# Kernel optimization log

Measured on AMD Instinct MI355X. Metric: run time of the kernel, lower is better.

Reference implementation:

```python
import jax, jax.numpy as jnp
import numpy as np

N = 1024   # num_nodes
D = 128    # embedding_size


def setup_inputs() -> dict:
    key = jax.random.key(0)
    k1, k2, k3 = jax.random.split(key, 3)
    z = jax.random.normal(k1, (N, D), dtype=jnp.float32)
    # torch.nn.Linear(2D, D): weight [D, 2D]; stored here as W1 [2D, D] for x @ W1
    W1 = jax.random.normal(k2, (2 * D, D), dtype=jnp.float32) * (1.0 / np.sqrt(2 * D))
    b1 = jnp.zeros((D,), dtype=jnp.float32)
    W2 = jax.random.normal(k3, (D, 1), dtype=jnp.float32) * (1.0 / np.sqrt(D))
    b2 = jnp.zeros((1,), dtype=jnp.float32)
    return {"z": z, "W1": W1, "b1": b1, "W2": W2, "b2": b2}


def reference(z, W1, b1, W2, b2):
    # Original: z_i = z.repeat_interleave(N) (i varies slowly),
    #           z_j = z.repeat(N)            (j varies fast),
    # q = Linear2(relu(Linear1(cat[z_i, z_j]))).squeeze()  -> shape [N*N]
    # Equivalent split-linear form (cat @ W1 == z_i @ W1[:D] + z_j @ W1[D:]):
    d = z.shape[1]
    pi = z @ W1[:d]          # [N, D] projection of left node
    pj = z @ W1[d:]          # [N, D] projection of right node
    h = jax.nn.relu(pi[:, None, :] + pj[None, :, :] + b1)  # [N, N, D]
    q = (h @ W2).squeeze(-1) + b2                          # [N, N]
    return q.reshape(-1)     # pair k = i*N + j, matching repeat_interleave/repeat order
```

## Files before the change

### kernel.cpp

```cpp
#include <hip/hip_runtime.h>


#define NN 1024
#define DD 128
#define TI 64
#define TJ 32
#define PAD 132

__global__ __launch_bounds__(256) void proj_kernel(
    const float* __restrict__ z,
    const float* __restrict__ W1,
    const float* __restrict__ b1,
    float* __restrict__ pic,
    float* __restrict__ pj)
{
    const int i0 = blockIdx.x * 4;
    const int t = threadIdx.x;
    const int half = t >> 7;
    const int d = t & (DD - 1);
    const float* __restrict__ Wcol = W1 + half * DD * DD + d;
    const float* __restrict__ z0 = z + i0 * DD;

    float a0 = 0.f, a1 = 0.f, a2 = 0.f, a3 = 0.f;
    #pragma unroll 8
    for (int k = 0; k < DD; ++k) {
        const float w = Wcol[k * DD];
        a0 = fmaf(z0[k], w, a0);
        a1 = fmaf(z0[DD + k], w, a1);
        a2 = fmaf(z0[2 * DD + k], w, a2);
        a3 = fmaf(z0[3 * DD + k], w, a3);
    }
    if (half == 0) {
        const float bb = b1[d];
        pic[(i0 + 0) * DD + d] = a0 + bb;
        pic[(i0 + 1) * DD + d] = a1 + bb;
        pic[(i0 + 2) * DD + d] = a2 + bb;
        pic[(i0 + 3) * DD + d] = a3 + bb;
    } else {
        pj[(i0 + 0) * DD + d] = a0;
        pj[(i0 + 1) * DD + d] = a1;
        pj[(i0 + 2) * DD + d] = a2;
        pj[(i0 + 3) * DD + d] = a3;
    }
}

__global__ __launch_bounds__(256, 2) void pair_kernel(
    const float* __restrict__ pic,
    const float* __restrict__ pj,
    const float* __restrict__ W2,
    const float* __restrict__ b2,
    float* __restrict__ out)
{
    __shared__ float a_s[TI * PAD];
    __shared__ float b_s[TJ * PAD];

    const int t  = threadIdx.x;
    const int bi = blockIdx.x;
    const int bj = blockIdx.y;

    const float4* __restrict__ srcA = (const float4*)(pic + bi * TI * DD);
    const float4* __restrict__ srcB = (const float4*)(pj + bj * TJ * DD);
    #pragma unroll
    for (int u = 0; u < 8; ++u) {
        int f   = t + 256 * u;
        int row = f >> 5;
        int c4  = f & 31;
        *(float4*)&a_s[row * PAD + c4 * 4] = srcA[f];
    }
    #pragma unroll
    for (int u = 0; u < 4; ++u) {
        int f   = t + 256 * u;
        int row = f >> 5;
        int c4  = f & 31;
        *(float4*)&b_s[row * PAD + c4 * 4] = srcB[f];
    }
    __syncthreads();

    const int tx = t & 15;
    const int ty = t >> 4;
    const float* ap = a_s + ty * PAD;
    const float* bp = b_s + tx * PAD;

    float acc[4][2];
    #pragma unroll
    for (int ii = 0; ii < 4; ++ii)
        #pragma unroll
        for (int jj = 0; jj < 2; ++jj) acc[ii][jj] = 0.f;

    #pragma unroll
    for (int d = 0; d < DD; d += 4) {
        const float4 w4 = *(const float4*)(W2 + d);
        float4 av[4], bv[2];
        #pragma unroll
        for (int ii = 0; ii < 4; ++ii) av[ii] = *(const float4*)(ap + ii * 16 * PAD + d);
        #pragma unroll
        for (int jj = 0; jj < 2; ++jj) bv[jj] = *(const float4*)(bp + jj * 16 * PAD + d);

        #pragma unroll
        for (int ii = 0; ii < 4; ++ii) {
            const float ax = av[ii].x, ay = av[ii].y, az = av[ii].z, aw = av[ii].w;
            #pragma unroll
            for (int jj = 0; jj < 2; ++jj) {
                acc[ii][jj] = fmaf(fmaxf(ax + bv[jj].x, 0.f), w4.x, acc[ii][jj]);
                acc[ii][jj] = fmaf(fmaxf(ay + bv[jj].y, 0.f), w4.y, acc[ii][jj]);
                acc[ii][jj] = fmaf(fmaxf(az + bv[jj].z, 0.f), w4.z, acc[ii][jj]);
                acc[ii][jj] = fmaf(fmaxf(aw + bv[jj].w, 0.f), w4.w, acc[ii][jj]);
            }
        }
    }

    const float bb = b2[0];
    #pragma unroll
    for (int ii = 0; ii < 4; ++ii) {
        const int i = bi * TI + ty + ii * 16;
        #pragma unroll
        for (int jj = 0; jj < 2; ++jj) {
            const int j = bj * TJ + tx + jj * 16;
            out[(size_t)i * NN + j] = acc[ii][jj] + bb;
        }
    }
}

extern "C" void kernel_launch(void* const* d_in, const int* in_sizes, int n_in,
                              void* d_out, int out_size, void* d_ws, size_t ws_size,
                              hipStream_t stream)
{
    const float* z  = (const float*)d_in[0];
    const float* W1 = (const float*)d_in[1];
    const float* b1 = (const float*)d_in[2];
    const float* W2 = (const float*)d_in[3];
    const float* b2 = (const float*)d_in[4];
    float* out = (float*)d_out;

    float* pic = (float*)d_ws;
    float* pj  = pic + NN * DD;

    proj_kernel<<<NN / 4, 256, 0, stream>>>(z, W1, b1, pic, pj);

    dim3 grid(NN / TI, NN / TJ);
    pair_kernel<<<grid, 256, 0, stream>>>(pic, pj, W2, b2, out);
}
```

Baseline: 79.54 us.

## Replace LDS-tiled pair kernel with register-streaming kernel over transposed pj

The right-node projection is written transposed so each thread reads its column j coalesced across d. The pair kernel drops shared-memory tiles: each thread owns one j and four i rows, streams pj values into registers in chunks, and reads pic rows and W2 as wave-uniform loads. This removes LDS traffic and barriers and raises occupancy, but each pj element is reused across only four rows, so global/L2 traffic grows substantially.

```diff
diff --git a/kernel.cpp b/kernel.cpp
--- a/kernel.cpp
+++ b/kernel.cpp
@@ -3,16 +3,15 @@
 
 #define NN 1024
 #define DD 128
-#define TI 64
-#define TJ 32
-#define PAD 132
+#define IT 4
+#define DC 32
 
 __global__ __launch_bounds__(256) void proj_kernel(
     const float* __restrict__ z,
     const float* __restrict__ W1,
     const float* __restrict__ b1,
     float* __restrict__ pic,
-    float* __restrict__ pj)
+    float* __restrict__ pjT)
 {
     const int i0 = blockIdx.x * 4;
     const int t = threadIdx.x;
@@ -37,88 +36,47 @@
         pic[(i0 + 2) * DD + d] = a2 + bb;
         pic[(i0 + 3) * DD + d] = a3 + bb;
     } else {
-        pj[(i0 + 0) * DD + d] = a0;
-        pj[(i0 + 1) * DD + d] = a1;
-        pj[(i0 + 2) * DD + d] = a2;
-        pj[(i0 + 3) * DD + d] = a3;
+        *(float4*)(pjT + (size_t)d * NN + i0) = make_float4(a0, a1, a2, a3);
     }
 }
 
-__global__ __launch_bounds__(256, 2) void pair_kernel(
+__global__ __launch_bounds__(256) void pair_kernel(
     const float* __restrict__ pic,
-    const float* __restrict__ pj,
+    const float* __restrict__ pjT,
     const float* __restrict__ W2,
     const float* __restrict__ b2,
     float* __restrict__ out)
 {
-    __shared__ float a_s[TI * PAD];
-    __shared__ float b_s[TJ * PAD];
+    const int t  = threadIdx.x;
+    const int j  = blockIdx.x * 256 + t;
+    const int i0 = blockIdx.y * IT;
 
-    const int t  = threadIdx.x;
-    const int bi = blockIdx.x;
-    const int bj = blockIdx.y;
+    float acc[IT];
+    #pragma unroll
+    for (int ii = 0; ii < IT; ++ii) acc[ii] = 0.f;
 
-    const float4* __restrict__ srcA = (const float4*)(pic + bi * TI * DD);
-    const float4* __restrict__ srcB = (const float4*)(pj + bj * TJ * DD);
-    #pragma unroll
-    for (int u = 0; u < 8; ++u) {
-        int f   = t + 256 * u;
-        int row = f >> 5;
-        int c4  = f & 31;
-        *(float4*)&a_s[row * PAD + c4 * 4] = srcA[f];
-    }
-    #pragma unroll
-    for (int u = 0; u < 4; ++u) {
-        int f   = t + 256 * u;
-        int row = f >> 5;
-        int c4  = f & 31;
-        *(float4*)&b_s[row * PAD + c4 * 4] = srcB[f];
-    }
-    __syncthreads();
+    const float* __restrict__ pr = pic + i0 * DD;
 
-    const int tx = t & 15;
-    const int ty = t >> 4;
-    const float* ap = a_s + ty * PAD;
-    const float* bp = b_s + tx * PAD;
-
-    float acc[4][2];
-    #pragma unroll
-    for (int ii = 0; ii < 4; ++ii)
+    for (int dc = 0; dc < DD; dc += DC) {
+        float pjv[DC];
         #pragma unroll
-        for (int jj = 0; jj < 2; ++jj) acc[ii][jj] = 0.f;
-
-    #pragma unroll
-    for (int d = 0; d < DD; d += 4) {
-        const float4 w4 = *(const float4*)(W2 + d);
-        float4 av[4], bv[2];
-        #pragma unroll
-        for (int ii = 0; ii < 4; ++ii) av[ii] = *(const float4*)(ap + ii * 16 * PAD + d);
-        #pragma unroll
-        for (int jj = 0; jj < 2; ++jj) bv[jj] = *(const float4*)(bp + jj * 16 * PAD + d);
+        for (int u = 0; u < DC; ++u)
+            pjv[u] = pjT[(size_t)(dc + u) * NN + j];
 
         #pragma unroll
-        for (int ii = 0; ii < 4; ++ii) {
-            const float ax = av[ii].x, ay = av[ii].y, az = av[ii].z, aw = av[ii].w;
+        for (int ii = 0; ii < IT; ++ii) {
             #pragma unroll
-            for (int jj = 0; jj < 2; ++jj) {
-                acc[ii][jj] = fmaf(fmaxf(ax + bv[jj].x, 0.f), w4.x, acc[ii][jj]);
-                acc[ii][jj] = fmaf(fmaxf(ay + bv[jj].y, 0.f), w4.y, acc[ii][jj]);
-                acc[ii][jj] = fmaf(fmaxf(az + bv[jj].z, 0.f), w4.z, acc[ii][jj]);
-                acc[ii][jj] = fmaf(fmaxf(aw + bv[jj].w, 0.f), w4.w, acc[ii][jj]);
+            for (int u = 0; u < DC; ++u) {
+                acc[ii] = fmaf(fmaxf(pr[ii * DD + dc + u] + pjv[u], 0.f),
+                               W2[dc + u], acc[ii]);
             }
         }
     }
 
     const float bb = b2[0];
     #pragma unroll
-    for (int ii = 0; ii < 4; ++ii) {
-        const int i = bi * TI + ty + ii * 16;
-        #pragma unroll
-        for (int jj = 0; jj < 2; ++jj) {
-            const int j = bj * TJ + tx + jj * 16;
-            out[(size_t)i * NN + j] = acc[ii][jj] + bb;
-        }
-    }
+    for (int ii = 0; ii < IT; ++ii)
+        out[(size_t)(i0 + ii) * NN + j] = acc[ii] + bb;
 }
 
 extern "C" void kernel_launch(void* const* d_in, const int* in_sizes, int n_in,
@@ -133,10 +91,10 @@
     float* out = (float*)d_out;
 
     float* pic = (float*)d_ws;
-    float* pj  = pic + NN * DD;
+    float* pjT = pic + NN * DD;
 
-    proj_kernel<<<NN / 4, 256, 0, stream>>>(z, W1, b1, pic, pj);
+    proj_kernel<<<NN / 4, 256, 0, stream>>>(z, W1, b1, pic, pjT);
 
-    dim3 grid(NN / TI, NN / TJ);
-    pair_kernel<<<grid, 256, 0, stream>>>(pic, pj, W2, b2, out);
+    dim3 grid(NN / 256, NN / IT);
+    pair_kernel<<<grid, 256, 0, stream>>>(pic, pjT, W2, b2, out);
 }
```

After: 83.76 us. 1.05x slower.
